# Performance work log

Measured on AMD Instinct MI355X. Metric: run time of the kernel, lower is better.

## Reference

```python
import jax, jax.numpy as jnp
import numpy as np
import math

NTOKEN, NINP, NHID, SEQ, BATCH = 33278, 400, 1150, 70, 16
ODE_STEPS = 8  # fixed-step RK4 over t in [0,1] (reference for the adaptive solver)


def lstm_layer(x, h0, c0, Wih, Whh, bih, bhh):
    # x: [S, B, in]; PyTorch gate order i, f, g, o
    def step(carry, xt):
        h, c = carry
        g = xt @ Wih.T + h @ Whh.T + bih + bhh
        i, f, gg, o = jnp.split(g, 4, axis=-1)
        c = jax.nn.sigmoid(f) * c + jax.nn.sigmoid(i) * jnp.tanh(gg)
        h = jax.nn.sigmoid(o) * jnp.tanh(c)
        return (h, c), h
    (hT, cT), ys = jax.lax.scan(step, (h0, c0), x)
    return ys, hT, cT


def cnf_delta_logp(E, cnf_W, cnf_b):
    # ODEnet: f(t,z) = relu(Linear(concat([t, z]))); exact divergence since
    # Jacobian diag = relu'(pre) * diag(Wx). Integrates dz/dt=f, d(dlogp)/dt=-div f.
    wt = cnf_W[:, 0]
    Wx = cnf_W[:, 1:]
    dWx = jnp.diag(Wx)

    def f(t, z):
        pre = z @ Wx.T + t * wt + cnf_b          # [ntoken, ninp]
        div = jnp.sum((pre > 0) * dWx, axis=-1)  # exact trace of df/dz
        return jax.nn.relu(pre), -div

    dt = 1.0 / ODE_STEPS

    def rk4(carry, t):
        z, dl = carry
        k1z, k1l = f(t, z)
        k2z, k2l = f(t + dt / 2, z + dt / 2 * k1z)
        k3z, k3l = f(t + dt / 2, z + dt / 2 * k2z)
        k4z, k4l = f(t + dt, z + dt * k3z)
        z = z + dt / 6 * (k1z + 2 * k2z + 2 * k3z + k4z)
        dl = dl + dt / 6 * (k1l + 2 * k2l + 2 * k3l + k4l)
        return (z, dl), None

    ts = jnp.arange(ODE_STEPS, dtype=E.dtype) * dt
    (zT, dl), _ = jax.lax.scan(rk4, (E, jnp.zeros(E.shape[0], E.dtype)), ts)
    return dl  # [ntoken]


def setup_inputs() -> dict:
    key = jax.random.key(0)
    ks = jax.random.split(key, 16)
    s = 0.1
    inp = {
        "tokens": jax.random.randint(ks[0], (SEQ, BATCH), 0, NTOKEN),
        "h0_0": jnp.zeros((BATCH, NHID), jnp.float32),
        "c0_0": jnp.zeros((BATCH, NHID), jnp.float32),
        "h0_1": jnp.zeros((BATCH, NHID), jnp.float32),
        "c0_1": jnp.zeros((BATCH, NHID), jnp.float32),
        "h0_2": jnp.zeros((BATCH, NINP), jnp.float32),
        "c0_2": jnp.zeros((BATCH, NINP), jnp.float32),
        "emb_W": jax.random.uniform(ks[1], (NTOKEN, NINP), jnp.float32, -s, s),
        "Wih0": jax.random.normal(ks[2], (4 * NHID, NINP), jnp.float32) * 0.02,
        "Whh0": jax.random.normal(ks[3], (4 * NHID, NHID), jnp.float32) * 0.02,
        "bih0": jnp.zeros((4 * NHID,), jnp.float32),
        "bhh0": jnp.zeros((4 * NHID,), jnp.float32),
        "Wih1": jax.random.normal(ks[4], (4 * NHID, NHID), jnp.float32) * 0.02,
        "Whh1": jax.random.normal(ks[5], (4 * NHID, NHID), jnp.float32) * 0.02,
        "bih1": jnp.zeros((4 * NHID,), jnp.float32),
        "bhh1": jnp.zeros((4 * NHID,), jnp.float32),
        "Wih2": jax.random.normal(ks[6], (4 * NINP, NHID), jnp.float32) * 0.02,
        "Whh2": jax.random.normal(ks[7], (4 * NINP, NINP), jnp.float32) * 0.02,
        "bih2": jnp.zeros((4 * NINP,), jnp.float32),
        "bhh2": jnp.zeros((4 * NINP,), jnp.float32),
        "cnf_W": jax.random.normal(ks[8], (NINP, NINP + 1), jnp.float32) * 0.05,
        "cnf_b": jnp.zeros((NINP,), jnp.float32),
    }
    return inp


def reference(tokens, h0_0, c0_0, h0_1, c0_1, h0_2, c0_2, emb_W,
              Wih0, Whh0, bih0, bhh0, Wih1, Whh1, bih1, bhh1,
              Wih2, Whh2, bih2, bhh2, cnf_W, cnf_b):
    # embedding (eval mode: all dropouts are identity)
    x = emb_W[tokens]                               # [S, B, ninp]
    x, h1, c1 = lstm_layer(x, h0_0, c0_0, Wih0, Whh0, bih0, bhh0)
    x, h2, c2 = lstm_layer(x, h0_1, c0_1, Wih1, Whh1, bih1, bhh1)
    x, h3, c3 = lstm_layer(x, h0_2, c0_2, Wih2, Whh2, bih2, bhh2)
    # nhidlast == ninp -> no latent projection
    h = x.reshape(SEQ * BATCH, NINP)

    # MVNLogProb vectorized: -0.5 ||E_v - h_i||^2 - k/2 log(2*pi)
    e2 = jnp.sum(emb_W * emb_W, axis=-1)            # [ntoken]
    h2n = jnp.sum(h * h, axis=-1, keepdims=True)    # [SB, 1]
    sq = e2[None, :] - 2.0 * (h @ emb_W.T) + h2n    # [SB, ntoken]
    log_pz0 = -0.5 * sq - (NINP / 2.0) * math.log(2.0 * math.pi)

    # CNF delta_logp is identical for every token position (loop-invariant)
    delta = cnf_delta_logp(emb_W, cnf_W, cnf_b)     # [ntoken]
    log_pz1 = log_pz0 - delta[None, :]

    prob = jax.nn.softmax(log_pz1, axis=-1)
    log_prob = jnp.log(prob + 1e-8)
    model_output = log_prob.reshape(SEQ, BATCH, NTOKEN)
    return model_output, h1, c1, h2, c2, h3, c3
```

## Files before the change

### kernel.cpp

```cpp
#include <hip/hip_runtime.h>
#include <hip/hip_bf16.h>
#include <math.h>

#define SEQL 70
#define NTOK 33278
#define ODE_STEPS 8
#define NBLK 242
#define CZS 418

typedef __attribute__((ext_vector_type(4))) float f32x4;
typedef __attribute__((ext_vector_type(8))) short s16x8;
typedef unsigned short u16;

__device__ __forceinline__ u16 f2b(float f) {
    union { float f; unsigned int u; } a; a.f = f;
    unsigned int u = a.u;
    return (u16)((u + 0x7FFFu + ((u >> 16) & 1u)) >> 16);
}
__device__ __forceinline__ float b2f(u16 s) {
    union { unsigned int u; float f; } a; a.u = ((unsigned int)s) << 16;
    return a.f;
}

__device__ __forceinline__ unsigned czoff(int row, int colb) {
    unsigned s = ((colb < 768 ? (row & 7) : (row & 3)) << 4);
    return (unsigned)(row * 832 + (colb ^ (int)s));
}

__global__ void cvt_pad_k(const float* __restrict__ src, u16* __restrict__ dst,
                          int G, int Nin, int Nop, int Kin, int Kp, int rs, int co) {
    size_t total = (size_t)G * Nop * Kp;
    for (size_t idx = (size_t)blockIdx.x * 256 + threadIdx.x; idx < total;
         idx += (size_t)gridDim.x * 256) {
        int k = (int)(idx % Kp);
        size_t t2 = idx / Kp;
        int j = (int)(t2 % Nop);
        int g = (int)(t2 / Nop);
        float v = 0.f;
        if (j < Nin && k < Kin) v = src[((size_t)g * Nin + j) * rs + co + k];
        dst[idx] = f2b(v);
    }
}

__global__ void bias_k(const float* __restrict__ bih, const float* __restrict__ bhh,
                       float* __restrict__ o, int Nin, int Nop) {
    int idx = blockIdx.x * 256 + threadIdx.x;
    if (idx >= 4 * Nop) return;
    int g = idx / Nop, j = idx % Nop;
    o[idx] = (j < Nin) ? (bih[g * Nin + j] + bhh[g * Nin + j]) : 0.f;
}

__global__ void wtdwx_k(const float* __restrict__ cw, float* __restrict__ wt,
                        float* __restrict__ dwx) {
    int i = blockIdx.x * 256 + threadIdx.x;
    if (i < 400) {
        wt[i]  = cw[(size_t)i * 401];
        dwx[i] = cw[(size_t)i * 401 + 1 + i];
    }
}

__global__ void h0cvt_k(const float* __restrict__ h0, u16* __restrict__ hb, int N, int Kp) {
    int idx = blockIdx.x * 256 + threadIdx.x;
    if (idx >= 16 * Kp) return;
    int b = idx / Kp, k = idx % Kp;
    hb[idx] = f2b(k < N ? h0[b * N + k] : 0.f);
}

__global__ void embed_k(const int* __restrict__ tok, const float* __restrict__ emb,
                        u16* __restrict__ x0) {
    int idx = blockIdx.x * 256 + threadIdx.x;
    if (idx >= 1152 * 416) return;
    int r = idx / 416, k = idx - r * 416;
    float v = 0.f;
    if (r < SEQL * 16 && k < 400) v = emb[(size_t)tok[r] * 400 + k];
    x0[idx] = f2b(v);
}

__global__ void rowsumsq_k(const float* __restrict__ X, float* __restrict__ o, int K) {
    int r = blockIdx.x;
    const float* xr = X + (size_t)r * K;
    int lane = threadIdx.x;
    float s = 0.f;
    for (int k = lane; k < K; k += 64) { float v = xr[k]; s += v * v; }
#pragma unroll
    for (int off = 1; off < 64; off <<= 1) s += __shfl_xor(s, off, 64);
    if (lane == 0) o[r] = s;
}

__global__ void ucomb_k(const float* __restrict__ e2, const float* __restrict__ dl,
                        float* __restrict__ u) {
    int i = blockIdx.x * 256 + threadIdx.x;
    if (i < NTOK) u[i] = -0.5f * e2[i] - dl[i];
}

__global__ void gemm_bt_k(const u16* __restrict__ A, const u16* __restrict__ B,
                          float* __restrict__ C, int Kp, int lda, int ldb, int ldc,
                          int Mreal, int Nreal, const float* __restrict__ uvec) {
    const int tid = threadIdx.x;
    const int wid = tid >> 6, lane = tid & 63;
    const int la = lane & 15, lk = (lane >> 4) * 8;
    const int m0 = blockIdx.y * 64 + wid * 16;
    const int n0 = blockIdx.x * 64;
    const f32x4 Z4 = {0.f, 0.f, 0.f, 0.f};
    f32x4 acc[4] = {Z4, Z4, Z4, Z4};
    const u16* Ar = A + (size_t)(m0 + la) * lda + lk;
    const u16* Br = B + (size_t)(n0 + la) * ldb + lk;
    for (int k = 0; k < Kp; k += 32) {
        s16x8 a = *(const s16x8*)(Ar + k);
#pragma unroll
        for (int nt = 0; nt < 4; ++nt) {
            s16x8 b = *(const s16x8*)(Br + (size_t)nt * 16 * ldb + k);
            acc[nt] = __builtin_amdgcn_mfma_f32_16x16x32_bf16(a, b, acc[nt], 0, 0, 0);
        }
    }
    const int mr = m0 + (lane >> 4) * 4;
#pragma unroll
    for (int nt = 0; nt < 4; ++nt) {
        int cc = n0 + nt * 16 + la;
        if (cc >= Nreal) continue;
        float uv = uvec ? uvec[cc] : 0.f;
#pragma unroll
        for (int r = 0; r < 4; ++r) {
            int rr = mr + r;
            if (rr < Mreal) C[(size_t)rr * ldc + cc] = acc[nt][r] + uv;
        }
    }
}

__device__ __forceinline__ void flatbar(int* cnt, int* gen, int nb, int iter) {
    __syncthreads();
    if (threadIdx.x == 0) {
        int old = __hip_atomic_fetch_add(cnt, 1, __ATOMIC_ACQ_REL, __HIP_MEMORY_SCOPE_AGENT);
        if ((old % nb) == nb - 1)
            __hip_atomic_fetch_add(gen, 1, __ATOMIC_ACQ_REL, __HIP_MEMORY_SCOPE_AGENT);
        while (__hip_atomic_load(gen, __ATOMIC_RELAXED, __HIP_MEMORY_SCOPE_AGENT) <= iter)
            __builtin_amdgcn_s_sleep(2);
        (void)__hip_atomic_load(gen, __ATOMIC_ACQUIRE, __HIP_MEMORY_SCOPE_AGENT);
    }
    __syncthreads();
}
__device__ __forceinline__ void waitgen(int* gen, int needed) {
    if (threadIdx.x == 0) {
        while (__hip_atomic_load(gen, __ATOMIC_RELAXED, __HIP_MEMORY_SCOPE_AGENT) < needed)
            __builtin_amdgcn_s_sleep(2);
        (void)__hip_atomic_load(gen, __ATOMIC_ACQUIRE, __HIP_MEMORY_SCOPE_AGENT);
    }
    __syncthreads();
}

__global__ __launch_bounds__(768, 3) void lstm_k(
    const float* __restrict__ c00, const float* __restrict__ c01,
    const float* __restrict__ c02,
    const u16* __restrict__ Whh0p, const u16* __restrict__ Wih1p,
    const u16* __restrict__ Whh1p, const u16* __restrict__ Wih2p,
    const u16* __restrict__ Whh2p,
    const float* __restrict__ xW0, const float* __restrict__ bias2v,
    const float* __restrict__ bias1v,
    u16* __restrict__ ys0s, u16* __restrict__ ys1s, u16* __restrict__ ys2s,
    float* __restrict__ oh1, float* __restrict__ oc1,
    float* __restrict__ oh2, float* __restrict__ oc2,
    float* __restrict__ oh3, float* __restrict__ oc3,
    int* __restrict__ bar)
{
    __shared__ __align__(16) char smem[162816];
    u16* wlds = (u16*)smem;
    float* gl = (float*)(smem + 147456);
    const int tid = threadIdx.x;
    const int bid = blockIdx.x;
    const int wv = tid >> 6, lane = tid & 63;
    const int la = lane & 15, lg = lane >> 4;

    int role, jb;
    if (bid < 72) { role = 0; jb = bid; }
    else if (bid < 216) { role = 1; jb = bid - 72; }
    else { role = 2; jb = bid - 216; }

    int* c0 = bar;        int* g0 = bar + 16;
    int* c1 = bar + 32;   int* g1 = bar + 48;
    int* c2 = bar + 64;   int* g2 = bar + 80;

    if (role == 0) {
        for (int s = tid; s < 4 * 36 * 64; s += 768) {
            int ln = s & 63, kt = (s >> 6) % 36, nt = s / (36 * 64);
            int row = nt * 1152 + jb * 16 + (ln & 15);
            int col = kt * 32 + (ln >> 4) * 8;
            *(s16x8*)(wlds + (size_t)s * 8) =
                *(const s16x8*)(Whh0p + (size_t)row * 1152 + col);
        }
    } else if (role == 1) {
        for (int s = tid; s < 2 * 72 * 64; s += 768) {
            int ln = s & 63, kt = (s >> 6) % 72, nt = s / (72 * 64);
            int lr = nt * 16 + (ln & 15);
            int row = (lr >> 3) * 1152 + jb * 8 + (lr & 7);
            int col8 = (ln >> 4) * 8;
            const u16* src = (kt < 36)
                ? Wih1p + (size_t)row * 1152 + kt * 32 + col8
                : Whh1p + (size_t)row * 1152 + (kt - 36) * 32 + col8;
            *(s16x8*)(wlds + (size_t)s * 8) = *(const s16x8*)src;
        }
    }
    __syncthreads();

    float c_reg = 0.f;
    for (int t = 0; t < SEQL; ++t) {
        if (role == 1) waitgen(g0, t + 1);
        else if (role == 2) waitgen(g1, t + 1);

        f32x4 acc = {0.f, 0.f, 0.f, 0.f};
        if (role == 0) {
            int nt = wv / 3, kg = wv - nt * 3;
            const u16* ar = ys0s + ((size_t)t * 16 + la) * 1152 + lg * 8;
            for (int kt = kg * 12; kt < kg * 12 + 12; ++kt) {
                s16x8 a = *(const s16x8*)(ar + kt * 32);
                s16x8 b = *(const s16x8*)(wlds + ((size_t)(nt * 36 + kt) * 64 + lane) * 8);
                acc = __builtin_amdgcn_mfma_f32_16x16x32_bf16(a, b, acc, 0, 0, 0);
            }
            *(f32x4*)(gl + wv * 320 + la * 20 + lg * 4) = acc;
        } else if (role == 1) {
            int nt = wv / 6, kg = wv - nt * 6;
            const u16* ax = ys0s + ((size_t)(t + 1) * 16 + la) * 1152 + lg * 8;
            const u16* ah = ys1s + ((size_t)t * 16 + la) * 1152 + lg * 8;
            for (int kt = kg * 12; kt < kg * 12 + 12; ++kt) {
                s16x8 a = (kt < 36) ? *(const s16x8*)(ax + kt * 32)
                                    : *(const s16x8*)(ah + (kt - 36) * 32);
                s16x8 b = *(const s16x8*)(wlds + ((size_t)(nt * 72 + kt) * 64 + lane) * 8);
                acc = __builtin_amdgcn_mfma_f32_16x16x32_bf16(a, b, acc, 0, 0, 0);
            }
            *(f32x4*)(gl + wv * 320 + la * 20 + lg * 4) = acc;
        } else {
            int nt = wv / 3, kg = wv - nt * 3;
            int k0 = (kg * 49) / 3, k1 = ((kg + 1) * 49) / 3;
            const u16* ax = ys1s + ((size_t)(t + 1) * 16 + la) * 1152 + lg * 8;
            const u16* ah = ys2s + ((size_t)t * 16 + la) * 416 + lg * 8;
            int wr = nt * 416 + jb * 16 + la;
            for (int kt = k0; kt < k1; ++kt) {
                s16x8 a, b;
                if (kt < 36) {
                    a = *(const s16x8*)(ax + kt * 32);
                    b = *(const s16x8*)(Wih2p + (size_t)wr * 1152 + kt * 32 + lg * 8);
                } else {
                    a = *(const s16x8*)(ah + (kt - 36) * 32);
                    b = *(const s16x8*)(Whh2p + (size_t)wr * 416 + (kt - 36) * 32 + lg * 8);
                }
                acc = __builtin_amdgcn_mfma_f32_16x16x32_bf16(a, b, acc, 0, 0, 0);
            }
            *(f32x4*)(gl + wv * 320 + la * 20 + lg * 4) = acc;
        }
        __syncthreads();
        if (role == 1) {
            if (tid < 128) {
                int u = tid & 7, tb = tid >> 3;
                int ug = jb * 8 + u;
                float gv[4];
#pragma unroll
                for (int g = 0; g < 4; ++g) {
                    int lr = g * 8 + u;
                    int nt = lr >> 4, li = lr & 15;
                    float s = 0.f;
#pragma unroll
                    for (int kg = 0; kg < 6; ++kg)
                        s += gl[(nt * 6 + kg) * 320 + li * 20 + tb];
                    gv[g] = s + bias1v[g * 1152 + ug];
                }
                float cprev = (t == 0) ? ((ug < 1150) ? c01[tb * 1150 + ug] : 0.f) : c_reg;
                float si = 1.f / (1.f + expf(-gv[0]));
                float sf = 1.f / (1.f + expf(-gv[1]));
                float so = 1.f / (1.f + expf(-gv[3]));
                float cn = sf * cprev + si * tanhf(gv[2]);
                float hn = so * tanhf(cn);
                c_reg = cn;
                if (ug < 1150) {
                    ys1s[((size_t)(t + 1) * 16 + tb) * 1152 + ug] = f2b(hn);
                    if (t == SEQL - 1) { oh2[tb * 1150 + ug] = hn; oc2[tb * 1150 + ug] = cn; }
                }
            }
        } else if (tid < 256) {
            int u = tid & 15, tb = tid >> 4;
            int ug = jb * 16 + u;
            float gv[4];
#pragma unroll
            for (int g = 0; g < 4; ++g) {
                float s = 0.f;
#pragma unroll
                for (int kg = 0; kg < 3; ++kg)
                    s += gl[(g * 3 + kg) * 320 + u * 20 + tb];
                gv[g] = s + ((role == 0)
                             ? xW0[((size_t)t * 16 + tb) * 4608 + g * 1152 + ug]
                             : bias2v[g * 416 + ug]);
            }
            int N = (role == 0) ? 1150 : 400;
            const float* c0i = (role == 0) ? c00 : c02;
            float cprev = (t == 0) ? ((ug < N) ? c0i[tb * N + ug] : 0.f) : c_reg;
            float si = 1.f / (1.f + expf(-gv[0]));
            float sf = 1.f / (1.f + expf(-gv[1]));
            float so = 1.f / (1.f + expf(-gv[3]));
            float cn = sf * cprev + si * tanhf(gv[2]);
            float hn = so * tanhf(cn);
            c_reg = cn;
            if (ug < N) {
                if (role == 0) {
                    ys0s[((size_t)(t + 1) * 16 + tb) * 1152 + ug] = f2b(hn);
                    if (t == SEQL - 1) { oh1[tb * 1150 + ug] = hn; oc1[tb * 1150 + ug] = cn; }
                } else {
                    ys2s[((size_t)(t + 1) * 16 + tb) * 416 + ug] = f2b(hn);
                    if (t == SEQL - 1) { oh3[tb * 400 + ug] = hn; oc3[tb * 400 + ug] = cn; }
                }
            }
        }
        if (role == 0) flatbar(c0, g0, 72, t);
        else if (role == 1) flatbar(c1, g1, 144, t);
        else flatbar(c2, g2, 26, t);
    }
}

__global__ __launch_bounds__(1024, 4) void cnf_k(const float* __restrict__ emb,
                                                 const u16* __restrict__ Wxp,
                                                 const float* __restrict__ wt,
                                                 const float* __restrict__ bv,
                                                 const float* __restrict__ dwx,
                                                 float* __restrict__ dl) {
    __shared__ float z0s[64 * CZS];
    __shared__ __align__(16) u16 zi[64 * 416];
    const int tid = threadIdx.x;
    const int m0 = blockIdx.x * 64;

    for (int idx = tid; idx < 64 * 416; idx += 1024) {
        int r = idx / 416, cc = idx - r * 416;
        int row = m0 + r;
        float v = (cc < 400 && row < NTOK) ? emb[(size_t)row * 400 + cc] : 0.f;
        z0s[r * CZS + cc] = v;
        *(u16*)((char*)zi + czoff(r, cc * 2)) = f2b(v);
    }

    const int wv = tid >> 6, lane = tid & 63;
    const int la = lane & 15, lg = lane >> 4;
    const int lk = lg * 8;
    const int tb0 = (wv * 25) >> 4;
    const int Qw = (((wv + 1) * 25) >> 4) - tb0;

    float wtq[2], bq[2], dwq[2];
#pragma unroll
    for (int q = 0; q < 2; ++q) {
        if (q < Qw) {
            int col = (tb0 + q) * 16 + la;
            wtq[q] = wt[col]; bq[q] = bv[col]; dwq[q] = dwx[col];
        } else { wtq[q] = 0.f; bq[q] = 0.f; dwq[q] = 0.f; }
    }
    __syncthreads();

    const float dt = 1.f / ODE_STEPS;
    const f32x4 Z4 = {0.f, 0.f, 0.f, 0.f};
    float Aacc[4][2][4];
#pragma unroll
    for (int m = 0; m < 4; ++m)
#pragma unroll
        for (int q = 0; q < 2; ++q)
#pragma unroll
            for (int r = 0; r < 4; ++r) Aacc[m][q][r] = 0.f;
    float divp[4][4];
#pragma unroll
    for (int m = 0; m < 4; ++m)
#pragma unroll
        for (int r = 0; r < 4; ++r) divp[m][r] = 0.f;

#pragma unroll 1
    for (int st = 0; st < ODE_STEPS; ++st) {
        float t0 = st * dt;
#pragma unroll 1
        for (int s = 0; s < 4; ++s) {
            float ts = t0 + ((s == 0) ? 0.f : (s == 3) ? dt : 0.5f * dt);
            float wgt = (s == 1 || s == 2) ? 2.f : 1.f;
            float cs = (s == 2) ? dt : 0.5f * dt;
            f32x4 pre[4][2];
#pragma unroll
            for (int m = 0; m < 4; ++m)
#pragma unroll
                for (int q = 0; q < 2; ++q) pre[m][q] = Z4;
#pragma unroll 1
            for (int kk = 0; kk < 13; ++kk) {
                s16x8 b[2];
#pragma unroll
                for (int q = 0; q < 2; ++q)
                    if (q < Qw)
                        b[q] = *(const s16x8*)(Wxp + (size_t)((tb0 + q) * 16 + la) * 416 +
                                               kk * 32 + lk);
#pragma unroll
                for (int m = 0; m < 4; ++m) {
                    int row = m * 16 + la;
                    s16x8 a = *(const s16x8*)((const char*)zi + czoff(row, kk * 64 + lg * 16));
#pragma unroll
                    for (int q = 0; q < 2; ++q)
                        if (q < Qw)
                            pre[m][q] = __builtin_amdgcn_mfma_f32_16x16x32_bf16(
                                a, b[q], pre[m][q], 0, 0, 0);
                }
            }
            __syncthreads();
#pragma unroll
            for (int m = 0; m < 4; ++m) {
#pragma unroll
                for (int q = 0; q < 2; ++q) {
                    if (q >= Qw) continue;
                    int col = (tb0 + q) * 16 + la;
#pragma unroll
                    for (int r = 0; r < 4; ++r) {
                        int row = m * 16 + lg * 4 + r;
                        float pv = pre[m][q][r] + ts * wtq[q] + bq[q];
                        float kz = fmaxf(pv, 0.f);
                        if (pv > 0.f) divp[m][r] += dwq[q] * wgt;
                        float An = Aacc[m][q][r] + wgt * kz;
                        float ev;
                        if (s < 3) {
                            Aacc[m][q][r] = An;
                            ev = z0s[row * CZS + col] + cs * kz;
                        } else {
                            float zn = z0s[row * CZS + col] + (dt / 6.f) * An;
                            z0s[row * CZS + col] = zn;
                            Aacc[m][q][r] = 0.f;
                            ev = zn;
                        }
                        *(u16*)((char*)zi + czoff(row, col * 2)) = f2b(ev);
                    }
                }
            }
            __syncthreads();
        }
    }

#pragma unroll
    for (int m = 0; m < 4; ++m)
#pragma unroll
        for (int r = 0; r < 4; ++r) {
            float v = divp[m][r];
            v += __shfl_xor(v, 1, 64);
            v += __shfl_xor(v, 2, 64);
            v += __shfl_xor(v, 4, 64);
            v += __shfl_xor(v, 8, 64);
            divp[m][r] = v;
        }
    float* dsc = (float*)zi;
    if (la == 0) {
#pragma unroll
        for (int m = 0; m < 4; ++m)
#pragma unroll
            for (int r = 0; r < 4; ++r)
                dsc[wv * 64 + m * 16 + lg * 4 + r] = divp[m][r];
    }
    __syncthreads();
    for (int row = tid; row < 64; row += 1024) {
        float s = 0.f;
#pragma unroll
        for (int w = 0; w < 16; ++w) s += dsc[w * 64 + row];
        if (m0 + row < NTOK) dl[m0 + row] = -(dt / 6.f) * s;
    }
}

__global__ void logsoftmax_k(float* __restrict__ L, int n) {
    const int row = blockIdx.x;
    float* R = L + (size_t)row * n;
    const int tid = threadIdx.x;
    float mx = -INFINITY, s = 0.f;
    for (int c = tid; c < n; c += 256) {
        float v = R[c];
        float nm = fmaxf(mx, v);
        s = s * expf(mx - nm) + expf(v - nm);
        mx = nm;
    }
#pragma unroll
    for (int off = 1; off < 64; off <<= 1) {
        float om = __shfl_xor(mx, off, 64);
        float os = __shfl_xor(s, off, 64);
        float nm = fmaxf(mx, om);
        s = s * expf(mx - nm) + os * expf(om - nm);
        mx = nm;
    }
    __shared__ float smx[4], ssm[4];
    if ((tid & 63) == 0) { smx[tid >> 6] = mx; ssm[tid >> 6] = s; }
    __syncthreads();
    float bm = fmaxf(fmaxf(smx[0], smx[1]), fmaxf(smx[2], smx[3]));
    float bs = ssm[0] * expf(smx[0] - bm) + ssm[1] * expf(smx[1] - bm) +
               ssm[2] * expf(smx[2] - bm) + ssm[3] * expf(smx[3] - bm);
    float lz = logf(bs);
    for (int c = tid; c < n; c += 256) {
        float v = R[c];
        R[c] = logf(expf(v - bm) + 1e-8f * bs) - lz;
    }
}

extern "C" void kernel_launch(void* const* d_in, const int* in_sizes, int n_in,
                              void* d_out, int out_size, void* d_ws, size_t ws_size,
                              hipStream_t stream) {
    const int*   tokens = (const int*)d_in[0];
    const float* h00 = (const float*)d_in[1];
    const float* c00 = (const float*)d_in[2];
    const float* h01 = (const float*)d_in[3];
    const float* c01 = (const float*)d_in[4];
    const float* h02 = (const float*)d_in[5];
    const float* c02 = (const float*)d_in[6];
    const float* embW = (const float*)d_in[7];
    const float* Wih0 = (const float*)d_in[8];
    const float* Whh0 = (const float*)d_in[9];
    const float* bih0 = (const float*)d_in[10];
    const float* bhh0 = (const float*)d_in[11];
    const float* Wih1 = (const float*)d_in[12];
    const float* Whh1 = (const float*)d_in[13];
    const float* bih1 = (const float*)d_in[14];
    const float* bhh1 = (const float*)d_in[15];
    const float* Wih2 = (const float*)d_in[16];
    const float* Whh2 = (const float*)d_in[17];
    const float* bih2 = (const float*)d_in[18];
    const float* bhh2 = (const float*)d_in[19];
    const float* cnfW = (const float*)d_in[20];
    const float* cnfb = (const float*)d_in[21];
    float* out = (float*)d_out;

    char* p = (char*)d_ws;
    auto alloc = [&](size_t bytes) -> void* {
        void* r = (void*)p;
        p += (bytes + 255) & ~(size_t)255;
        return r;
    };
    u16*   emb_p = (u16*)alloc((size_t)33280 * 416 * 2);
    u16*   x0    = (u16*)alloc((size_t)1152 * 416 * 2);
    u16*   ys0s  = (u16*)alloc((size_t)1136 * 1152 * 2);
    u16*   ys1s  = (u16*)alloc((size_t)1136 * 1152 * 2);
    u16*   ys2s  = (u16*)alloc((size_t)1184 * 416 * 2);
    float* xW    = (float*)alloc((size_t)1120 * 4608 * 4);
    u16*   Wih0p = (u16*)alloc((size_t)4608 * 416 * 2);
    u16*   Whh0p = (u16*)alloc((size_t)4608 * 1152 * 2);
    u16*   Wih1p = (u16*)alloc((size_t)4608 * 1152 * 2);
    u16*   Whh1p = (u16*)alloc((size_t)4608 * 1152 * 2);
    u16*   Wih2p = (u16*)alloc((size_t)1664 * 1152 * 2);
    u16*   Whh2p = (u16*)alloc((size_t)1664 * 416 * 2);
    float* bias0 = (float*)alloc((size_t)4608 * 4);
    float* bias1 = (float*)alloc((size_t)4608 * 4);
    float* bias2 = (float*)alloc((size_t)1664 * 4);
    u16*   Wxp   = (u16*)alloc((size_t)416 * 416 * 2);
    float* wtv   = (float*)alloc((size_t)400 * 4);
    float* dwx   = (float*)alloc((size_t)400 * 4);
    float* dl    = (float*)alloc((size_t)NTOK * 4);
    float* e2    = (float*)alloc((size_t)NTOK * 4);
    float* uvec  = (float*)alloc((size_t)NTOK * 4);
    int*   bar   = (int*)alloc(4096);

    size_t OM = (size_t)SEQL * 16 * NTOK;
    float* oh1 = out + OM;
    float* oc1 = oh1 + 16 * 1150;
    float* oh2 = oc1 + 16 * 1150;
    float* oc2 = oh2 + 16 * 1150;
    float* oh3 = oc2 + 16 * 1150;
    float* oc3 = oh3 + 16 * 400;

    hipMemsetAsync(bar, 0, 4096, stream);
    hipMemsetAsync(ys0s, 0, (size_t)1136 * 1152 * 2, stream);
    hipMemsetAsync(ys1s, 0, (size_t)1136 * 1152 * 2, stream);
    hipMemsetAsync(ys2s, 0, (size_t)1184 * 416 * 2, stream);

    cvt_pad_k<<<2048, 256, 0, stream>>>(Wih0, Wih0p, 4, 1150, 1152, 400, 416, 400, 0);
    cvt_pad_k<<<2048, 256, 0, stream>>>(Whh0, Whh0p, 4, 1150, 1152, 1150, 1152, 1150, 0);
    cvt_pad_k<<<2048, 256, 0, stream>>>(Wih1, Wih1p, 4, 1150, 1152, 1150, 1152, 1150, 0);
    cvt_pad_k<<<2048, 256, 0, stream>>>(Whh1, Whh1p, 4, 1150, 1152, 1150, 1152, 1150, 0);
    cvt_pad_k<<<2048, 256, 0, stream>>>(Wih2, Wih2p, 4, 400, 416, 1150, 1152, 1150, 0);
    cvt_pad_k<<<2048, 256, 0, stream>>>(Whh2, Whh2p, 4, 400, 416, 400, 416, 400, 0);
    cvt_pad_k<<<2048, 256, 0, stream>>>(embW, emb_p, 1, 33278, 33280, 400, 416, 400, 0);
    cvt_pad_k<<<2048, 256, 0, stream>>>(cnfW, Wxp, 1, 400, 416, 400, 416, 401, 1);
    bias_k<<<(4 * 1152 + 255) / 256, 256, 0, stream>>>(bih0, bhh0, bias0, 1150, 1152);
    bias_k<<<(4 * 1152 + 255) / 256, 256, 0, stream>>>(bih1, bhh1, bias1, 1150, 1152);
    bias_k<<<(4 * 416 + 255) / 256, 256, 0, stream>>>(bih2, bhh2, bias2, 400, 416);
    wtdwx_k<<<2, 256, 0, stream>>>(cnfW, wtv, dwx);
    rowsumsq_k<<<NTOK, 64, 0, stream>>>(embW, e2, 400);

    h0cvt_k<<<(16 * 1152 + 255) / 256, 256, 0, stream>>>(h00, ys0s, 1150, 1152);
    h0cvt_k<<<(16 * 1152 + 255) / 256, 256, 0, stream>>>(h01, ys1s, 1150, 1152);
    h0cvt_k<<<(16 * 416 + 255) / 256, 256, 0, stream>>>(h02, ys2s, 400, 416);

    cnf_k<<<520, 1024, 0, stream>>>(embW, Wxp, wtv, cnfb, dwx, dl);
    ucomb_k<<<(NTOK + 255) / 256, 256, 0, stream>>>(e2, dl, uvec);

    embed_k<<<(1152 * 416 + 255) / 256, 256, 0, stream>>>(tokens, embW, x0);
    gemm_bt_k<<<dim3(72, 18), 256, 0, stream>>>(x0, Wih0p, xW, 416, 416, 416, 4608,
                                                1120, 4608, bias0);

    lstm_k<<<NBLK, 768, 0, stream>>>(
        c00, c01, c02, Whh0p, Wih1p, Whh1p, Wih2p, Whh2p,
        xW, bias2, bias1, ys0s, ys1s, ys2s,
        oh1, oc1, oh2, oc2, oh3, oc3, bar);

    gemm_bt_k<<<dim3(520, 18), 256, 0, stream>>>(ys2s + (size_t)16 * 416, emb_p, out,
                                                 416, 416, 416, NTOK, 1120, NTOK, uvec);
    logsoftmax_k<<<1120, 256, 0, stream>>>(out, NTOK);
}
```

Measured before the change: 2.993 ms.

## Replace counter-based grid barriers with per-block flags and coherent loads

Replaces the atomic counter/generation barriers between LSTM layer roles with per-block progress flags, each padded to its own slot. Threads in parallel poll exactly the producer blocks they depend on. Activations are written and read with system-coherent (sc0 sc1) global accesses that bypass caches. A-operand loads are batched into registers before the MFMA loops so memory latency overlaps. The goal is to cut atomic serialization and barrier latency on the recurrent critical path, at the cost of more polling traffic and uncached loads.

Result: slower. 3.403 ms (+13.7%).

```diff
diff --git a/kernel.cpp b/kernel.cpp
--- a/kernel.cpp
+++ b/kernel.cpp
@@ -25,6 +25,29 @@
 __device__ __forceinline__ unsigned czoff(int row, int colb) {
     unsigned s = ((colb < 768 ? (row & 7) : (row & 3)) << 4);
     return (unsigned)(row * 832 + (colb ^ (int)s));
+}
+
+__device__ __forceinline__ int load_flag(const int* p) {
+    int v;
+    asm volatile("global_load_dword %0, %1, off sc0 sc1\ns_waitcnt vmcnt(0)"
+                 : "=v"(v) : "v"(p) : "memory");
+    return v;
+}
+__device__ __forceinline__ void store_flag(int* p, int v) {
+    asm volatile("global_store_dword %0, %1, off sc0 sc1" :: "v"(p), "v"(v) : "memory");
+}
+__device__ __forceinline__ s16x8 ld128_coh(const u16* p) {
+    s16x8 v;
+    asm volatile("global_load_dwordx4 %0, %1, off sc0 sc1" : "=v"(v) : "v"(p));
+    return v;
+}
+__device__ __forceinline__ void st16_coh(u16* p, u16 v) {
+    unsigned w = v;
+    asm volatile("global_store_short %0, %1, off sc0 sc1" :: "v"(p), "v"(w) : "memory");
+}
+__device__ __forceinline__ void drain_vm() {
+    asm volatile("s_waitcnt vmcnt(0)" ::: "memory");
+    __builtin_amdgcn_sched_barrier(0);
 }
 
 __global__ void cvt_pad_k(const float* __restrict__ src, u16* __restrict__ dst,
@@ -125,27 +148,6 @@
             if (rr < Mreal) C[(size_t)rr * ldc + cc] = acc[nt][r] + uv;
         }
     }
-}
-
-__device__ __forceinline__ void flatbar(int* cnt, int* gen, int nb, int iter) {
-    __syncthreads();
-    if (threadIdx.x == 0) {
-        int old = __hip_atomic_fetch_add(cnt, 1, __ATOMIC_ACQ_REL, __HIP_MEMORY_SCOPE_AGENT);
-        if ((old % nb) == nb - 1)
-            __hip_atomic_fetch_add(gen, 1, __ATOMIC_ACQ_REL, __HIP_MEMORY_SCOPE_AGENT);
-        while (__hip_atomic_load(gen, __ATOMIC_RELAXED, __HIP_MEMORY_SCOPE_AGENT) <= iter)
-            __builtin_amdgcn_s_sleep(2);
-        (void)__hip_atomic_load(gen, __ATOMIC_ACQUIRE, __HIP_MEMORY_SCOPE_AGENT);
-    }
-    __syncthreads();
-}
-__device__ __forceinline__ void waitgen(int* gen, int needed) {
-    if (threadIdx.x == 0) {
-        while (__hip_atomic_load(gen, __ATOMIC_RELAXED, __HIP_MEMORY_SCOPE_AGENT) < needed)
-            __builtin_amdgcn_s_sleep(2);
-        (void)__hip_atomic_load(gen, __ATOMIC_ACQUIRE, __HIP_MEMORY_SCOPE_AGENT);
-    }
-    __syncthreads();
 }
 
 __global__ __launch_bounds__(768, 3) void lstm_k(
@@ -174,10 +176,7 @@
     if (bid < 72) { role = 0; jb = bid; }
     else if (bid < 216) { role = 1; jb = bid - 72; }
     else { role = 2; jb = bid - 216; }
-
-    int* c0 = bar;        int* g0 = bar + 16;
-    int* c1 = bar + 32;   int* g1 = bar + 48;
-    int* c2 = bar + 64;   int* g2 = bar + 80;
+    const int flagIdx = (role == 0) ? jb : (role == 1) ? 72 + jb : 216 + jb;
 
     if (role == 0) {
         for (int s = tid; s < 4 * 36 * 64; s += 768) {
@@ -203,28 +202,51 @@
 
     float c_reg = 0.f;
     for (int t = 0; t < SEQL; ++t) {
-        if (role == 1) waitgen(g0, t + 1);
-        else if (role == 2) waitgen(g1, t + 1);
+        if (role == 0) {
+            if (tid < 72)
+                while (load_flag(bar + tid * 16) < t) __builtin_amdgcn_s_sleep(2);
+        } else if (role == 1) {
+            if (tid < 72)
+                while (load_flag(bar + tid * 16) < t + 1) __builtin_amdgcn_s_sleep(2);
+            else if (tid >= 128 && tid < 272)
+                while (load_flag(bar + (72 + tid - 128) * 16) < t) __builtin_amdgcn_s_sleep(2);
+        } else {
+            if (tid < 144)
+                while (load_flag(bar + (72 + tid) * 16) < t + 1) __builtin_amdgcn_s_sleep(2);
+            else if (tid >= 192 && tid < 218)
+                while (load_flag(bar + (216 + tid - 192) * 16) < t) __builtin_amdgcn_s_sleep(2);
+        }
+        __syncthreads();
 
         f32x4 acc = {0.f, 0.f, 0.f, 0.f};
         if (role == 0) {
             int nt = wv / 3, kg = wv - nt * 3;
-            const u16* ar = ys0s + ((size_t)t * 16 + la) * 1152 + lg * 8;
-            for (int kt = kg * 12; kt < kg * 12 + 12; ++kt) {
-                s16x8 a = *(const s16x8*)(ar + kt * 32);
-                s16x8 b = *(const s16x8*)(wlds + ((size_t)(nt * 36 + kt) * 64 + lane) * 8);
-                acc = __builtin_amdgcn_mfma_f32_16x16x32_bf16(a, b, acc, 0, 0, 0);
+            const u16* ab = ys0s + ((size_t)t * 16 + la) * 1152 + lg * 8 + (size_t)kg * 384;
+            s16x8 a0[12];
+#pragma unroll
+            for (int i = 0; i < 12; ++i) a0[i] = ld128_coh(ab + i * 32);
+            drain_vm();
+#pragma unroll
+            for (int i = 0; i < 12; ++i) {
+                s16x8 b = *(const s16x8*)(wlds +
+                          ((size_t)(nt * 36 + kg * 12 + i) * 64 + lane) * 8);
+                acc = __builtin_amdgcn_mfma_f32_16x16x32_bf16(a0[i], b, acc, 0, 0, 0);
             }
             *(f32x4*)(gl + wv * 320 + la * 20 + lg * 4) = acc;
         } else if (role == 1) {
             int nt = wv / 6, kg = wv - nt * 6;
-            const u16* ax = ys0s + ((size_t)(t + 1) * 16 + la) * 1152 + lg * 8;
-            const u16* ah = ys1s + ((size_t)t * 16 + la) * 1152 + lg * 8;
-            for (int kt = kg * 12; kt < kg * 12 + 12; ++kt) {
-                s16x8 a = (kt < 36) ? *(const s16x8*)(ax + kt * 32)
-                                    : *(const s16x8*)(ah + (kt - 36) * 32);
-                s16x8 b = *(const s16x8*)(wlds + ((size_t)(nt * 72 + kt) * 64 + lane) * 8);
-                acc = __builtin_amdgcn_mfma_f32_16x16x32_bf16(a, b, acc, 0, 0, 0);
+            const u16* ab = (kg < 3)
+                ? ys0s + ((size_t)(t + 1) * 16 + la) * 1152 + lg * 8 + (size_t)kg * 384
+                : ys1s + ((size_t)t * 16 + la) * 1152 + lg * 8 + (size_t)(kg * 12 - 36) * 32;
+            s16x8 a1[12];
+#pragma unroll
+            for (int i = 0; i < 12; ++i) a1[i] = ld128_coh(ab + i * 32);
+            drain_vm();
+#pragma unroll
+            for (int i = 0; i < 12; ++i) {
+                s16x8 b = *(const s16x8*)(wlds +
+                          ((size_t)(nt * 72 + kg * 12 + i) * 64 + lane) * 8);
+                acc = __builtin_amdgcn_mfma_f32_16x16x32_bf16(a1[i], b, acc, 0, 0, 0);
             }
             *(f32x4*)(gl + wv * 320 + la * 20 + lg * 4) = acc;
         } else {
@@ -232,21 +254,29 @@
             int k0 = (kg * 49) / 3, k1 = ((kg + 1) * 49) / 3;
             const u16* ax = ys1s + ((size_t)(t + 1) * 16 + la) * 1152 + lg * 8;
             const u16* ah = ys2s + ((size_t)t * 16 + la) * 416 + lg * 8;
+            s16x8 a2[17];
+#pragma unroll
+            for (int i = 0; i < 17; ++i) {
+                int kt = k0 + i;
+                if (kt < k1)
+                    a2[i] = ld128_coh(kt < 36 ? ax + kt * 32 : ah + (kt - 36) * 32);
+            }
+            drain_vm();
             int wr = nt * 416 + jb * 16 + la;
-            for (int kt = k0; kt < k1; ++kt) {
-                s16x8 a, b;
-                if (kt < 36) {
-                    a = *(const s16x8*)(ax + kt * 32);
-                    b = *(const s16x8*)(Wih2p + (size_t)wr * 1152 + kt * 32 + lg * 8);
-                } else {
-                    a = *(const s16x8*)(ah + (kt - 36) * 32);
-                    b = *(const s16x8*)(Whh2p + (size_t)wr * 416 + (kt - 36) * 32 + lg * 8);
+#pragma unroll
+            for (int i = 0; i < 17; ++i) {
+                int kt = k0 + i;
+                if (kt < k1) {
+                    s16x8 b = (kt < 36)
+                        ? *(const s16x8*)(Wih2p + (size_t)wr * 1152 + kt * 32 + lg * 8)
+                        : *(const s16x8*)(Whh2p + (size_t)wr * 416 + (kt - 36) * 32 + lg * 8);
+                    acc = __builtin_amdgcn_mfma_f32_16x16x32_bf16(a2[i], b, acc, 0, 0, 0);
                 }
-                acc = __builtin_amdgcn_mfma_f32_16x16x32_bf16(a, b, acc, 0, 0, 0);
             }
             *(f32x4*)(gl + wv * 320 + la * 20 + lg * 4) = acc;
         }
         __syncthreads();
+
         if (role == 1) {
             if (tid < 128) {
                 int u = tid & 7, tb = tid >> 3;
@@ -270,9 +300,10 @@
                 float hn = so * tanhf(cn);
                 c_reg = cn;
                 if (ug < 1150) {
-                    ys1s[((size_t)(t + 1) * 16 + tb) * 1152 + ug] = f2b(hn);
+                    st16_coh(ys1s + ((size_t)(t + 1) * 16 + tb) * 1152 + ug, f2b(hn));
                     if (t == SEQL - 1) { oh2[tb * 1150 + ug] = hn; oc2[tb * 1150 + ug] = cn; }
                 }
+                drain_vm();
             }
         } else if (tid < 256) {
             int u = tid & 15, tb = tid >> 4;
@@ -299,17 +330,17 @@
             c_reg = cn;
             if (ug < N) {
                 if (role == 0) {
-                    ys0s[((size_t)(t + 1) * 16 + tb) * 1152 + ug] = f2b(hn);
+                    st16_coh(ys0s + ((size_t)(t + 1) * 16 + tb) * 1152 + ug, f2b(hn));
                     if (t == SEQL - 1) { oh1[tb * 1150 + ug] = hn; oc1[tb * 1150 + ug] = cn; }
                 } else {
-                    ys2s[((size_t)(t + 1) * 16 + tb) * 416 + ug] = f2b(hn);
+                    st16_coh(ys2s + ((size_t)(t + 1) * 16 + tb) * 416 + ug, f2b(hn));
                     if (t == SEQL - 1) { oh3[tb * 400 + ug] = hn; oc3[tb * 400 + ug] = cn; }
                 }
             }
-        }
-        if (role == 0) flatbar(c0, g0, 72, t);
-        else if (role == 1) flatbar(c1, g1, 144, t);
-        else flatbar(c2, g2, 26, t);
+            drain_vm();
+        }
+        __syncthreads();
+        if (tid == 0) store_flag(bar + flagIdx * 16, t + 1);
     }
 }
 
@@ -541,7 +572,7 @@
     float* dl    = (float*)alloc((size_t)NTOK * 4);
     float* e2    = (float*)alloc((size_t)NTOK * 4);
     float* uvec  = (float*)alloc((size_t)NTOK * 4);
-    int*   bar   = (int*)alloc(4096);
+    int*   bar   = (int*)alloc(16384);
 
     size_t OM = (size_t)SEQL * 16 * NTOK;
     float* oh1 = out + OM;
@@ -551,7 +582,7 @@
     float* oh3 = oc2 + 16 * 1150;
     float* oc3 = oh3 + 16 * 400;
 
-    hipMemsetAsync(bar, 0, 4096, stream);
+    hipMemsetAsync(bar, 0, 16384, stream);
     hipMemsetAsync(ys0s, 0, (size_t)1136 * 1152 * 2, stream);
     hipMemsetAsync(ys1s, 0, (size_t)1136 * 1152 * 2, stream);
     hipMemsetAsync(ys2s, 0, (size_t)1184 * 416 * 2, stream);
```
